# Performance work log

Measured on AMD Instinct MI355X. Metric: run time of the kernel, lower is better.

The kernel has to match this reference:

```python
import jax, jax.numpy as jnp
import numpy as np

DIM = 256

def setup_inputs() -> dict:
    key = jax.random.key(0)
    ks = jax.random.split(key, 7)
    s = 1.0 / np.sqrt(DIM)
    x = jax.random.normal(ks[0], (16, DIM, 32, 32), dtype=jnp.float32)
    proj_w = jax.random.uniform(ks[1], (DIM, DIM), jnp.float32, -s, s)
    proj_b = jax.random.uniform(ks[2], (DIM,), jnp.float32, -s, s)
    w1 = jax.random.uniform(ks[3], (DIM, DIM), jnp.float32, -s, s)
    b1 = jax.random.uniform(ks[4], (DIM,), jnp.float32, -s, s)
    w2 = jax.random.uniform(ks[5], (DIM, DIM), jnp.float32, -s, s)
    b2 = jax.random.uniform(ks[6], (DIM,), jnp.float32, -s, s)
    return {"x": x, "proj_w": proj_w, "proj_b": proj_b, "w1": w1, "b1": b1, "w2": w2, "b2": b2}

def reference(x, proj_w, proj_b, w1, b1, w2, b2):
    B, C, H, W = x.shape
    # nodes: [B, N, C] with N = H*W
    nodes = x.reshape(B, C, H * W).transpose(0, 2, 1)
    q = nodes @ proj_w.T + proj_b                      # [B,N,C]
    scores = jnp.einsum('bnc,bmc->bnm', q, q) / jnp.sqrt(jnp.float32(C))
    attn = jax.nn.softmax(scores, axis=-1)             # [B,N,N]
    agg = jnp.einsum('bnm,bmc->bnc', attn, nodes)      # [B,N,C]
    h = jax.nn.gelu(agg @ w1.T + b1, approximate=False)
    out = h @ w2.T + b2                                # [B,N,C]
    return x + out.transpose(0, 2, 1).reshape(B, C, H, W)
```

## Files before the change

### kernel.cpp

```cpp
#include <hip/hip_runtime.h>
#include <stdint.h>

typedef unsigned short u16;
typedef __attribute__((ext_vector_type(8))) short short8;
typedef __attribute__((ext_vector_type(4))) float f32x4;

#define NB    16
#define DIM   256
#define NTOK  1024

__device__ __forceinline__ u16 f2b(float f) {
    union { float f; uint32_t u; } v; v.f = f;
    uint32_t u = v.u;
    u += 0x7fffu + ((u >> 16) & 1u);
    return (u16)(u >> 16);
}
__device__ __forceinline__ uint32_t pack2(float a, float b) {
    return (uint32_t)f2b(a) | ((uint32_t)f2b(b) << 16);
}
__device__ __forceinline__ f32x4 mfma16(short8 a, short8 b, f32x4 c) {
    return __builtin_amdgcn_mfma_f32_16x16x32_bf16(a, b, c, 0, 0, 0);
}
__device__ __forceinline__ short8 ld8(const u16* p) {
    return *reinterpret_cast<const short8*>(p);
}
__device__ __forceinline__ void gl_lds(const u16* g, u16* l) {
    __builtin_amdgcn_global_load_lds((const __attribute__((address_space(1))) void*)g,
                                     (__attribute__((address_space(3))) void*)l, 16, 0, 0);
}

__global__ __launch_bounds__(256) void pack_kernel(const float* __restrict__ x,
                                                   u16* __restrict__ xbf,
                                                   u16* __restrict__ nodes) {
    __shared__ float tile[64][65];
    int tid = threadIdx.x;
    int blk = blockIdx.x;
    int b  = blk >> 6;
    int t  = blk & 63;
    int c0 = (t >> 4) << 6;
    int n0 = (t & 15) << 6;
    const float* xb = x + (size_t)b * (DIM * NTOK);
    u16* xbb = xbf + (size_t)b * (DIM * NTOK);
#pragma unroll
    for (int i = 0; i < 16; i++) {
        int idx = i * 256 + tid;
        int cl = idx >> 6, nl = idx & 63;
        float f = xb[(c0 + cl) * NTOK + n0 + nl];
        tile[cl][nl] = f;
        xbb[(c0 + cl) * NTOK + n0 + nl] = f2b(f);
    }
    __syncthreads();
#pragma unroll
    for (int i = 0; i < 16; i++) {
        int idx = i * 256 + tid;
        int nl = idx >> 6, cl = idx & 63;
        nodes[(size_t)(b * NTOK + n0 + nl) * DIM + c0 + cl] = f2b(tile[cl][nl]);
    }
}

__global__ __launch_bounds__(256) void wconv_kernel(const float* __restrict__ a,
                                                    const float* __restrict__ b,
                                                    const float* __restrict__ c,
                                                    u16* __restrict__ o) {
    int i = blockIdx.x * 256 + threadIdx.x;
    const float* s = (i < 65536) ? a : (i < 131072) ? b : c;
    o[i] = f2b(s[i & 65535]);
}

__global__ __launch_bounds__(256) void proj_kernel(const u16* __restrict__ nodes,
                                                   const u16* __restrict__ wbf,
                                                   const float* __restrict__ pb,
                                                   u16* __restrict__ qb) {
    int lane = threadIdx.x & 63;
    int w = threadIdx.x >> 6;
    int lo = lane & 15, hi = lane >> 4;
    int ch = blockIdx.x & 1;
    int row0 = (blockIdx.x >> 1) * 64 + w * 16;
    const u16* arow = nodes + (size_t)(row0 + lo) * DIM + hi * 8;
    f32x4 acc[8];
#pragma unroll
    for (int i = 0; i < 8; i++) acc[i] = (f32x4){0.f, 0.f, 0.f, 0.f};
#pragma unroll
    for (int t = 0; t < 8; t++) {
        short8 a = ld8(arow + t * 32);
#pragma unroll
        for (int nf = 0; nf < 8; nf++) {
            short8 bfr = ld8(wbf + ((ch * 8 + nf) * 16 + lo) * DIM + t * 32 + hi * 8);
            acc[nf] = mfma16(a, bfr, acc[nf]);
        }
    }
#pragma unroll
    for (int nf = 0; nf < 8; nf++) {
        int col = (ch * 8 + nf) * 16 + lo;
        float bias = pb[col];
#pragma unroll
        for (int r = 0; r < 4; r++) {
            int row = row0 + hi * 4 + r;
            qb[(size_t)row * DIM + col] = f2b(acc[nf][r] + bias);
        }
    }
}

__global__ __launch_bounds__(256) void attn_kernel(const u16* __restrict__ qb,
                                                   const u16* __restrict__ xbf,
                                                   u16* __restrict__ agg) {
    __shared__ u16 kls[2][16384];
    __shared__ u16 vls[2][16384];

    int lane = threadIdx.x & 63;
    int w = threadIdx.x >> 6;
    int lo = lane & 15, hi = lane >> 4;
    int b  = blockIdx.x & 15;
    int qt = blockIdx.x >> 4;
    int q0 = qt * 64 + w * 16;
    const u16* qbb = qb  + (size_t)b * (NTOK * DIM);
    const u16* xbb = xbf + (size_t)b * (DIM * NTOK);

    int kOff[8], vOff[8];
#pragma unroll
    for (int ii = 0; ii < 8; ii++) {
        int i = w * 8 + ii;
        int krow = 2 * i + (lane >> 5);
        int kslot = (lane & 31) ^ (krow & 7);
        kOff[ii] = krow * DIM + kslot * 8;
        int vc = 8 * i + (lane >> 3);
        int vs = (lane & 7) ^ (vc & 7);
        vOff[ii] = vc * NTOK + vs * 8;
    }

    short8 bq[8];
#pragma unroll
    for (int t = 0; t < 8; t++)
        bq[t] = ld8(qbb + (size_t)(q0 + lo) * DIM + t * 32 + hi * 8);

    f32x4 acc[16];
#pragma unroll
    for (int i = 0; i < 16; i++) acc[i] = (f32x4){0.f, 0.f, 0.f, 0.f};
    float m = -1e30f, ell = 0.f;
    const float C1 = 0.0625f * 1.44269504f;
    const float THR = 11.5f;

#pragma unroll
    for (int ii = 0; ii < 8; ii++) {
        gl_lds(qbb + kOff[ii],        &kls[0][(w * 8 + ii) * 512]);
        gl_lds(xbb + vOff[ii],        &vls[0][(w * 8 + ii) * 512]);
    }
    __syncthreads();

    for (int tt = 0; tt < 16; tt++) {
        int buf = tt & 1;
        if (tt < 15) {
            int kvE = (tt + 1) * 64;
#pragma unroll
            for (int ii = 0; ii < 8; ii++) {
                gl_lds(qbb + kvE * DIM + kOff[ii], &kls[buf ^ 1][(w * 8 + ii) * 512]);
                gl_lds(xbb + kvE       + vOff[ii], &vls[buf ^ 1][(w * 8 + ii) * 512]);
            }
        }
        const u16* kb = &kls[buf][0];
        const u16* vb = &vls[buf][0];

        f32x4 sfr[4];
#pragma unroll
        for (int s = 0; s < 4; s++) sfr[s] = (f32x4){0.f, 0.f, 0.f, 0.f};
#pragma unroll
        for (int t = 0; t < 8; t++) {
            int sl = ((t * 4 + hi) ^ (lo & 7)) * 8;
#pragma unroll
            for (int s = 0; s < 4; s++) {
                short8 a = ld8(kb + (s * 16 + lo) * DIM + sl);
                sfr[s] = mfma16(a, bq[t], sfr[s]);
            }
        }

        float p[16];
        float pm = -1e30f;
#pragma unroll
        for (int s = 0; s < 4; s++)
#pragma unroll
            for (int r = 0; r < 4; r++) {
                p[s * 4 + r] = sfr[s][r] * C1;
                pm = fmaxf(pm, p[s * 4 + r]);
            }
        pm = fmaxf(pm, __shfl_xor(pm, 16));
        pm = fmaxf(pm, __shfl_xor(pm, 32));
        if (!__all(pm <= m + THR)) {
            float mnew = fmaxf(m, pm);
            float sc = exp2f(m - mnew);
            ell *= sc;
#pragma unroll
            for (int i = 0; i < 16; i++) {
                acc[i][0] *= sc; acc[i][1] *= sc; acc[i][2] *= sc; acc[i][3] *= sc;
            }
            m = mnew;
        }
        float psum = 0.f;
#pragma unroll
        for (int i = 0; i < 16; i++) {
            p[i] = exp2f(p[i] - m);
            psum += p[i];
        }
        psum += __shfl_xor(psum, 16);
        psum += __shfl_xor(psum, 32);
        ell += psum;

        short8 pfrag[2];
#pragma unroll
        for (int h = 0; h < 2; h++) {
            uint32_t pl0 = pack2(p[h * 8 + 0], p[h * 8 + 1]);
            uint32_t ph0 = pack2(p[h * 8 + 2], p[h * 8 + 3]);
            uint32_t pl1 = pack2(p[h * 8 + 4], p[h * 8 + 5]);
            uint32_t ph1 = pack2(p[h * 8 + 6], p[h * 8 + 7]);
            int srcA = ((hi & 1) << 5) | lo;
            int srcB = srcA + 16;
            uint32_t w0a = __shfl(pl0, srcA), w0b = __shfl(pl1, srcA);
            uint32_t w1a = __shfl(ph0, srcA), w1b = __shfl(ph1, srcA);
            uint32_t w2a = __shfl(pl0, srcB), w2b = __shfl(pl1, srcB);
            uint32_t w3a = __shfl(ph0, srcB), w3b = __shfl(ph1, srcB);
            bool sel = (hi >= 2);
            union { uint32_t u[4]; short8 v; } pu;
            pu.u[0] = sel ? w0b : w0a;
            pu.u[1] = sel ? w1b : w1a;
            pu.u[2] = sel ? w2b : w2a;
            pu.u[3] = sel ? w3b : w3a;
            pfrag[h] = pu.v;
        }

#pragma unroll
        for (int h = 0; h < 2; h++) {
            int sl = ((h * 4 + hi) ^ (lo & 7)) * 8;
#pragma unroll
            for (int mf = 0; mf < 16; mf++) {
                short8 a = ld8(vb + (mf * 16 + lo) * 64 + sl);
                acc[mf] = mfma16(a, pfrag[h], acc[mf]);
            }
        }
        __syncthreads();
    }

    float rinv = 1.f / ell;
#pragma unroll
    for (int mf = 0; mf < 16; mf++) {
        ushort4 st;
        st.x = f2b(acc[mf][0] * rinv);
        st.y = f2b(acc[mf][1] * rinv);
        st.z = f2b(acc[mf][2] * rinv);
        st.w = f2b(acc[mf][3] * rinv);
        *reinterpret_cast<ushort4*>(agg + (size_t)(b * NTOK + q0 + lo) * DIM + mf * 16 + hi * 4) = st;
    }
}

__global__ __launch_bounds__(512) void ffn_kernel(const u16* __restrict__ agg,
                                                  const u16* __restrict__ wbf,
                                                  const float* __restrict__ b1,
                                                  const float* __restrict__ b2,
                                                  const float* __restrict__ x,
                                                  float* __restrict__ out) {
    __shared__ u16 hl[64][264];
    int lane = threadIdx.x & 63;
    int w = threadIdx.x >> 6;
    int wr = w & 3, wc = w >> 2;
    int lo = lane & 15, hi = lane >> 4;
    int row0 = blockIdx.x * 64;
    int rw = row0 + wr * 16;
    const u16* w1b = wbf + 65536;
    const u16* w2b = wbf + 131072;

    f32x4 acc[8];
#pragma unroll
    for (int i = 0; i < 8; i++) acc[i] = (f32x4){0.f, 0.f, 0.f, 0.f};
    const u16* arow = agg + (size_t)(rw + lo) * DIM + hi * 8;
#pragma unroll
    for (int t = 0; t < 8; t++) {
        short8 a = ld8(arow + t * 32);
#pragma unroll
        for (int nf = 0; nf < 8; nf++) {
            short8 bfr = ld8(w1b + ((wc * 8 + nf) * 16 + lo) * DIM + t * 32 + hi * 8);
            acc[nf] = mfma16(a, bfr, acc[nf]);
        }
    }
#pragma unroll
    for (int nf = 0; nf < 8; nf++) {
        int f = (wc * 8 + nf) * 16 + lo;
        float bias = b1[f];
#pragma unroll
        for (int r = 0; r < 4; r++) {
            float v = acc[nf][r] + bias;
            float g = 0.5f * v * (1.f + erff(v * 0.70710678f));
            hl[wr * 16 + hi * 4 + r][f] = f2b(g);
        }
    }
    __syncthreads();

    f32x4 acc2[8];
#pragma unroll
    for (int i = 0; i < 8; i++) acc2[i] = (f32x4){0.f, 0.f, 0.f, 0.f};
#pragma unroll
    for (int t = 0; t < 8; t++) {
        short8 bh = ld8(&hl[wr * 16 + lo][t * 32 + hi * 8]);
#pragma unroll
        for (int mf = 0; mf < 8; mf++) {
            short8 a = ld8(w2b + ((wc * 8 + mf) * 16 + lo) * DIM + t * 32 + hi * 8);
            acc2[mf] = mfma16(a, bh, acc2[mf]);
        }
    }
    int bidx = row0 >> 10;
    int n = (rw & 1023) + lo;
#pragma unroll
    for (int mf = 0; mf < 8; mf++) {
#pragma unroll
        for (int r = 0; r < 4; r++) {
            int co = (wc * 8 + mf) * 16 + hi * 4 + r;
            size_t addr = (size_t)bidx * (DIM * NTOK) + (size_t)co * NTOK + n;
            out[addr] = acc2[mf][r] + b2[co] + x[addr];
        }
    }
}

extern "C" void kernel_launch(void* const* d_in, const int* in_sizes, int n_in,
                              void* d_out, int out_size, void* d_ws, size_t ws_size,
                              hipStream_t stream) {
    const float* x      = (const float*)d_in[0];
    const float* proj_w = (const float*)d_in[1];
    const float* proj_b = (const float*)d_in[2];
    const float* w1     = (const float*)d_in[3];
    const float* b1     = (const float*)d_in[4];
    const float* w2     = (const float*)d_in[5];
    const float* b2     = (const float*)d_in[6];
    float* out = (float*)d_out;

    u16* xbf   = (u16*)d_ws;
    u16* nodes = xbf   + 4194304;
    u16* qb    = nodes + 4194304;
    u16* agg   = qb    + 4194304;
    u16* wbf   = agg   + 4194304;

    pack_kernel <<<1024, 256, 0, stream>>>(x, xbf, nodes);
    wconv_kernel<<<768,  256, 0, stream>>>(proj_w, w1, w2, wbf);
    proj_kernel <<<512,  256, 0, stream>>>(nodes, wbf, proj_b, qb);
    attn_kernel <<<256,  256, 0, stream>>>(qb, xbf, agg);
    ffn_kernel  <<<256,  512, 0, stream>>>(agg, wbf, b1, b2, x, out);
}
```

Before: 116.6 us.

## Use four-stage 32-key LDS pipeline with vmcnt waits and MFMA priority

Result: slower. 130.3 us (+11.8%).

```diff
diff --git a/kernel.cpp b/kernel.cpp
--- a/kernel.cpp
+++ b/kernel.cpp
@@ -104,8 +104,8 @@
 __global__ __launch_bounds__(256) void attn_kernel(const u16* __restrict__ qb,
                                                    const u16* __restrict__ xbf,
                                                    u16* __restrict__ agg) {
-    __shared__ u16 kls[2][16384];
-    __shared__ u16 vls[2][16384];
+    __shared__ u16 kls[4][32 * 256];
+    __shared__ u16 vls[4][256 * 32];
 
     int lane = threadIdx.x & 63;
     int w = threadIdx.x >> 6;
@@ -116,16 +116,15 @@
     const u16* qbb = qb  + (size_t)b * (NTOK * DIM);
     const u16* xbb = xbf + (size_t)b * (DIM * NTOK);
 
-    int kOff[8], vOff[8];
-#pragma unroll
-    for (int ii = 0; ii < 8; ii++) {
-        int i = w * 8 + ii;
-        int krow = 2 * i + (lane >> 5);
-        int kslot = (lane & 31) ^ (krow & 7);
-        kOff[ii] = krow * DIM + kslot * 8;
-        int vc = 8 * i + (lane >> 3);
-        int vs = (lane & 7) ^ (vc & 7);
-        vOff[ii] = vc * NTOK + vs * 8;
+    int kOff[4], vOff[4], kDst[4], vDst[4];
+#pragma unroll
+    for (int i = 0; i < 4; i++) {
+        int kr = w * 8 + i * 2 + (lane >> 5);
+        kOff[i] = kr * DIM + ((lane & 31) ^ (kr & 7)) * 8;
+        kDst[i] = (w * 8 + i * 2) * 256;
+        int vc = w * 64 + i * 16 + (lane >> 2);
+        vOff[i] = vc * NTOK + ((lane & 3) ^ ((vc >> 2) & 3)) * 8;
+        vDst[i] = (w * 64 + i * 16) * 32;
     }
 
     short8 bq[8];
@@ -141,47 +140,51 @@
     const float THR = 11.5f;
 
 #pragma unroll
-    for (int ii = 0; ii < 8; ii++) {
-        gl_lds(qbb + kOff[ii],        &kls[0][(w * 8 + ii) * 512]);
-        gl_lds(xbb + vOff[ii],        &vls[0][(w * 8 + ii) * 512]);
-    }
-    __syncthreads();
-
-    for (int tt = 0; tt < 16; tt++) {
-        int buf = tt & 1;
-        if (tt < 15) {
-            int kvE = (tt + 1) * 64;
-#pragma unroll
-            for (int ii = 0; ii < 8; ii++) {
-                gl_lds(qbb + kvE * DIM + kOff[ii], &kls[buf ^ 1][(w * 8 + ii) * 512]);
-                gl_lds(xbb + kvE       + vOff[ii], &vls[buf ^ 1][(w * 8 + ii) * 512]);
+    for (int T = 0; T < 3; T++) {
+        int base = T * 32;
+#pragma unroll
+        for (int i = 0; i < 4; i++) {
+            gl_lds(qbb + base * DIM + kOff[i], &kls[T][kDst[i]]);
+            gl_lds(xbb + base       + vOff[i], &vls[T][vDst[i]]);
+        }
+    }
+
+    for (int tt = 0; tt < 32; tt++) {
+        if (tt <= 29)      asm volatile("s_waitcnt vmcnt(16)" ::: "memory");
+        else if (tt == 30) asm volatile("s_waitcnt vmcnt(8)"  ::: "memory");
+        else               asm volatile("s_waitcnt vmcnt(0)"  ::: "memory");
+        __builtin_amdgcn_s_barrier();
+        if (tt + 3 < 32) {
+            int base = (tt + 3) * 32;
+            int B = (tt + 3) & 3;
+#pragma unroll
+            for (int i = 0; i < 4; i++) {
+                gl_lds(qbb + base * DIM + kOff[i], &kls[B][kDst[i]]);
+                gl_lds(xbb + base       + vOff[i], &vls[B][vDst[i]]);
             }
         }
-        const u16* kb = &kls[buf][0];
-        const u16* vb = &vls[buf][0];
-
-        f32x4 sfr[4];
-#pragma unroll
-        for (int s = 0; s < 4; s++) sfr[s] = (f32x4){0.f, 0.f, 0.f, 0.f};
+        const u16* kb = &kls[tt & 3][0];
+        const u16* vb = &vls[tt & 3][0];
+
+        f32x4 s0 = (f32x4){0.f, 0.f, 0.f, 0.f};
+        f32x4 s1 = (f32x4){0.f, 0.f, 0.f, 0.f};
+        __builtin_amdgcn_s_setprio(1);
 #pragma unroll
         for (int t = 0; t < 8; t++) {
             int sl = ((t * 4 + hi) ^ (lo & 7)) * 8;
-#pragma unroll
-            for (int s = 0; s < 4; s++) {
-                short8 a = ld8(kb + (s * 16 + lo) * DIM + sl);
-                sfr[s] = mfma16(a, bq[t], sfr[s]);
-            }
-        }
-
-        float p[16];
+            s0 = mfma16(ld8(kb + lo * 256 + sl),        bq[t], s0);
+            s1 = mfma16(ld8(kb + (16 + lo) * 256 + sl), bq[t], s1);
+        }
+        __builtin_amdgcn_s_setprio(0);
+
+        float p0[4], p1[4];
         float pm = -1e30f;
 #pragma unroll
-        for (int s = 0; s < 4; s++)
-#pragma unroll
-            for (int r = 0; r < 4; r++) {
-                p[s * 4 + r] = sfr[s][r] * C1;
-                pm = fmaxf(pm, p[s * 4 + r]);
-            }
+        for (int r = 0; r < 4; r++) {
+            p0[r] = s0[r] * C1;
+            p1[r] = s1[r] * C1;
+            pm = fmaxf(pm, fmaxf(p0[r], p1[r]));
+        }
         pm = fmaxf(pm, __shfl_xor(pm, 16));
         pm = fmaxf(pm, __shfl_xor(pm, 32));
         if (!__all(pm <= m + THR)) {
@@ -196,46 +199,39 @@
         }
         float psum = 0.f;
 #pragma unroll
-        for (int i = 0; i < 16; i++) {
-            p[i] = exp2f(p[i] - m);
-            psum += p[i];
+        for (int r = 0; r < 4; r++) {
+            p0[r] = exp2f(p0[r] - m);
+            p1[r] = exp2f(p1[r] - m);
+            psum += p0[r] + p1[r];
         }
         psum += __shfl_xor(psum, 16);
         psum += __shfl_xor(psum, 32);
         ell += psum;
 
-        short8 pfrag[2];
-#pragma unroll
-        for (int h = 0; h < 2; h++) {
-            uint32_t pl0 = pack2(p[h * 8 + 0], p[h * 8 + 1]);
-            uint32_t ph0 = pack2(p[h * 8 + 2], p[h * 8 + 3]);
-            uint32_t pl1 = pack2(p[h * 8 + 4], p[h * 8 + 5]);
-            uint32_t ph1 = pack2(p[h * 8 + 6], p[h * 8 + 7]);
-            int srcA = ((hi & 1) << 5) | lo;
-            int srcB = srcA + 16;
-            uint32_t w0a = __shfl(pl0, srcA), w0b = __shfl(pl1, srcA);
-            uint32_t w1a = __shfl(ph0, srcA), w1b = __shfl(ph1, srcA);
-            uint32_t w2a = __shfl(pl0, srcB), w2b = __shfl(pl1, srcB);
-            uint32_t w3a = __shfl(ph0, srcB), w3b = __shfl(ph1, srcB);
-            bool sel = (hi >= 2);
-            union { uint32_t u[4]; short8 v; } pu;
-            pu.u[0] = sel ? w0b : w0a;
-            pu.u[1] = sel ? w1b : w1a;
-            pu.u[2] = sel ? w2b : w2a;
-            pu.u[3] = sel ? w3b : w3a;
-            pfrag[h] = pu.v;
-        }
-
-#pragma unroll
-        for (int h = 0; h < 2; h++) {
-            int sl = ((h * 4 + hi) ^ (lo & 7)) * 8;
-#pragma unroll
-            for (int mf = 0; mf < 16; mf++) {
-                short8 a = ld8(vb + (mf * 16 + lo) * 64 + sl);
-                acc[mf] = mfma16(a, pfrag[h], acc[mf]);
-            }
-        }
-        __syncthreads();
+        uint32_t pl0 = pack2(p0[0], p0[1]), ph0 = pack2(p0[2], p0[3]);
+        uint32_t pl1 = pack2(p1[0], p1[1]), ph1 = pack2(p1[2], p1[3]);
+        int srcA = ((hi & 1) << 5) | lo;
+        int srcB = srcA + 16;
+        uint32_t w0a = __shfl(pl0, srcA), w0b = __shfl(pl1, srcA);
+        uint32_t w1a = __shfl(ph0, srcA), w1b = __shfl(ph1, srcA);
+        uint32_t w2a = __shfl(pl0, srcB), w2b = __shfl(pl1, srcB);
+        uint32_t w3a = __shfl(ph0, srcB), w3b = __shfl(ph1, srcB);
+        bool sel = (hi >= 2);
+        union { uint32_t u[4]; short8 v; } pu;
+        pu.u[0] = sel ? w0b : w0a;
+        pu.u[1] = sel ? w1b : w1a;
+        pu.u[2] = sel ? w2b : w2a;
+        pu.u[3] = sel ? w3b : w3a;
+        short8 pfrag = pu.v;
+
+        int vsl = (hi ^ ((lo >> 2) & 3)) * 8;
+        __builtin_amdgcn_s_setprio(1);
+#pragma unroll
+        for (int mf = 0; mf < 16; mf++) {
+            short8 a = ld8(vb + (mf * 16 + lo) * 32 + vsl);
+            acc[mf] = mfma16(a, pfrag, acc[mf]);
+        }
+        __builtin_amdgcn_s_setprio(0);
     }
 
     float rinv = 1.f / ell;
```
